# Kernel tuning notes

Measured on AMD Instinct MI355X. Metric: run time of the kernel, lower is better.

Reference implementation:

```python
import jax, jax.numpy as jnp
import numpy as np

N = 50000   # nodes
E = 800000  # edges
H = 3       # attention heads
IN_F = 128
HID = 128
NUM_CLASSES = 6
GAT_SLOPE = 0.2   # DGL GATConv internal leaky_relu slope
ACT_SLOPE = 0.01  # nn.LeakyReLU default


def setup_inputs() -> dict:
    key = jax.random.key(0)
    ks = jax.random.split(key, 24)
    s = 0.05
    inp = {
        "in_feat": jax.random.normal(ks[0], (N, IN_F), jnp.float32),
        "src": jax.random.randint(ks[1], (E,), 0, N, jnp.int32),
        "dst": jax.random.randint(ks[2], (E,), 0, N, jnp.int32),
        # GATConv 1: W (IN_F, H*HID), attn vectors (H, HID), bias (H*HID)
        "W1": jax.random.normal(ks[3], (IN_F, H * HID), jnp.float32) * s,
        "al1": jax.random.normal(ks[4], (H, HID), jnp.float32) * s,
        "ar1": jax.random.normal(ks[5], (H, HID), jnp.float32) * s,
        "b1": jnp.zeros((H * HID,), jnp.float32),
        # GATConv 2
        "W2": jax.random.normal(ks[6], (HID, H * HID), jnp.float32) * s,
        "al2": jax.random.normal(ks[7], (H, HID), jnp.float32) * s,
        "ar2": jax.random.normal(ks[8], (H, HID), jnp.float32) * s,
        "b2": jnp.zeros((H * HID,), jnp.float32),
    }
    # Dense MLP head lin1..lin4 (HID->HID) and lin5 (HID->NUM_CLASSES)
    for i in range(1, 5):
        inp[f"lw{i}"] = jax.random.normal(ks[8 + 2 * i], (HID, HID), jnp.float32) * s
        inp[f"lb{i}"] = jnp.zeros((HID,), jnp.float32)
    inp["lw5"] = jax.random.normal(ks[20], (HID, NUM_CLASSES), jnp.float32) * s
    inp["lb5"] = jnp.zeros((NUM_CLASSES,), jnp.float32)
    return inp


def gat_conv(x, src, dst, W, al, ar, b):
    # x: (N, F_in) -> out: (N, H, HID)
    h = (x @ W).reshape(N, H, HID)
    el = jnp.einsum('nhf,hf->nh', h, al)  # (N, H)
    er = jnp.einsum('nhf,hf->nh', h, ar)
    e = jax.nn.leaky_relu(el[src] + er[dst], GAT_SLOPE)  # (E, H)
    # edge softmax over incoming edges of each dst node
    m = jax.ops.segment_max(e, dst, num_segments=N)
    m = jnp.where(jnp.isfinite(m), m, 0.0)
    ex = jnp.exp(e - m[dst])
    denom = jax.ops.segment_sum(ex, dst, num_segments=N)
    alpha = ex / (denom[dst] + 1e-9)  # (E, H)
    out = jax.ops.segment_sum(alpha[:, :, None] * h[src], dst, num_segments=N)
    return out + b.reshape(1, H, HID)


def reference(in_feat, src, dst, W1, al1, ar1, b1, W2, al2, ar2, b2,
              lw1, lb1, lw2, lb2, lw3, lb3, lw4, lb4, lw5, lb5):
    act = lambda x: jax.nn.leaky_relu(x, ACT_SLOPE)
    h = act(gat_conv(in_feat, src, dst, W1, al1, ar1, b1)).mean(axis=1)
    h = act(gat_conv(h, src, dst, W2, al2, ar2, b2)).mean(axis=1)
    h = act(h @ lw1 + lb1)
    h = act(h @ lw2 + lb2)
    h = act(h @ lw3 + lb3)
    h = act(h @ lw4 + lb4)
    return h @ lw5 + lb5
```

## Files before the change

### kernel.cpp

```cpp
#include <hip/hip_runtime.h>
#include <hip/hip_bf16.h>


typedef __attribute__((ext_vector_type(8))) short short8;
typedef __attribute__((ext_vector_type(4))) float float4v;

__device__ inline short f2bf(float x) {
    union { float f; unsigned u; } v; v.f = x;
    unsigned r = v.u + 0x7FFFu + ((v.u >> 16) & 1u);
    return (short)(r >> 16);
}
__device__ inline float bf2f(short b) {
    union { float f; unsigned u; } v;
    v.u = ((unsigned)(unsigned short)b) << 16;
    return v.f;
}
__device__ inline short8 zero8() { short8 z = {0,0,0,0,0,0,0,0}; return z; }

#define BM 128
#define BN 128
#define BK 32
#define LSTR 40
#define MSTR 136
#define MROWS 64

__global__ void prep_kernel(
    const float* __restrict__ in_feat, short* __restrict__ P1h,
    short* __restrict__ P1l, int n4, int cb, int wb,
    const int* __restrict__ dst, int* __restrict__ cnt, int E,
    const float* __restrict__ w1, const float* __restrict__ w2,
    const float* __restrict__ m1, const float* __restrict__ m2,
    const float* __restrict__ m3, const float* __restrict__ m4,
    const float* __restrict__ w5,
    short* __restrict__ w1h, short* __restrict__ w1l,
    short* __restrict__ w2h, short* __restrict__ w2l,
    short* __restrict__ m1h, short* __restrict__ m1l,
    short* __restrict__ m2h, short* __restrict__ m2l,
    short* __restrict__ m3h, short* __restrict__ m3l,
    short* __restrict__ m4h, short* __restrict__ m4l,
    short* __restrict__ w5h, short* __restrict__ w5l)
{
    int blk = blockIdx.x;
    if (blk < cb) {
        int i = blk * 256 + threadIdx.x;
        if (i >= n4) return;
        float4 v = *(const float4*)(in_feat + (size_t)i * 4);
        float xs[4] = {v.x, v.y, v.z, v.w};
        short hs[4], ls[4];
        #pragma unroll
        for (int j = 0; j < 4; ++j) {
            hs[j] = f2bf(xs[j]);
            ls[j] = f2bf(xs[j] - bf2f(hs[j]));
        }
        *(uint2*)(P1h + (size_t)i * 4) = *(uint2*)hs;
        *(uint2*)(P1l + (size_t)i * 4) = *(uint2*)ls;
    } else if (blk < cb + wb) {
        int j = (blk - cb) * 256 + threadIdx.x;
        const float* src; short* th; short* tl; int Nc, base;
        if      (j < 49152)  { src = w1; th = w1h; tl = w1l; Nc = 384; base = 0; }
        else if (j < 98304)  { src = w2; th = w2h; tl = w2l; Nc = 384; base = 49152; }
        else if (j < 114688) { src = m1; th = m1h; tl = m1l; Nc = 128; base = 98304; }
        else if (j < 131072) { src = m2; th = m2h; tl = m2l; Nc = 128; base = 114688; }
        else if (j < 147456) { src = m3; th = m3h; tl = m3l; Nc = 128; base = 131072; }
        else if (j < 163840) { src = m4; th = m4h; tl = m4l; Nc = 128; base = 147456; }
        else if (j < 164608) { src = w5; th = w5h; tl = w5l; Nc = 6;   base = 163840; }
        else return;
        int i = j - base;
        int k = i / Nc, c = i - k * Nc;
        float v = src[i];
        short h = f2bf(v);
        th[(size_t)c * 128 + k] = h;
        tl[(size_t)c * 128 + k] = f2bf(v - bf2f(h));
    } else {
        int e = (blk - cb - wb) * 256 + threadIdx.x;
        if (e < E) atomicAdd(&cnt[dst[e]], 1);
    }
}

__global__ __launch_bounds__(256) void gemm_mfma(
    const short* __restrict__ Ahi, const short* __restrict__ Alo,
    const short* __restrict__ Bth, const short* __restrict__ Btl,
    const float* __restrict__ bias,
    float* __restrict__ Cf, short* __restrict__ Chi, short* __restrict__ Clo,
    float* __restrict__ el, float* __restrict__ er,
    const float* __restrict__ al, const float* __restrict__ ar,
    int M, int Nc, int flags)
{
    __shared__ short Ah[BM * LSTR], Al_[BM * LSTR];
    __shared__ short Bh[BN * LSTR], Bl_[BN * LSTR];

    int tid = threadIdx.x, lane = tid & 63, wave = tid >> 6;
    int l15 = lane & 15, q = lane >> 4;
    int rowBase = blockIdx.y * BM, colBase = blockIdx.x * BN;

    float4v acc[2][8];
    #pragma unroll
    for (int mt = 0; mt < 2; ++mt)
        #pragma unroll
        for (int nt = 0; nt < 8; ++nt)
            acc[mt][nt] = (float4v){0.f, 0.f, 0.f, 0.f};

    for (int k0 = 0; k0 < 128; k0 += BK) {
        #pragma unroll
        for (int s = 0; s < 2; ++s) {
            int c = tid + s * 256;
            int r = c >> 2, kq = (c & 3) * 8;
            int gr = rowBase + r;
            short8 vh = zero8(), vl = zero8();
            if (gr < M) {
                vh = *(const short8*)(Ahi + (size_t)gr * 128 + k0 + kq);
                vl = *(const short8*)(Alo + (size_t)gr * 128 + k0 + kq);
            }
            *(short8*)&Ah[r * LSTR + kq]  = vh;
            *(short8*)&Al_[r * LSTR + kq] = vl;
            int gc = colBase + r;
            short8 wh = zero8(), wl = zero8();
            if (gc < Nc) {
                wh = *(const short8*)(Bth + (size_t)gc * 128 + k0 + kq);
                wl = *(const short8*)(Btl + (size_t)gc * 128 + k0 + kq);
            }
            *(short8*)&Bh[r * LSTR + kq]  = wh;
            *(short8*)&Bl_[r * LSTR + kq] = wl;
        }
        __syncthreads();

        short8 aH[2], aL2[2];
        #pragma unroll
        for (int mt = 0; mt < 2; ++mt) {
            int off = (wave * 32 + mt * 16 + l15) * LSTR + q * 8;
            aH[mt]  = *(short8*)&Ah[off];
            aL2[mt] = *(short8*)&Al_[off];
        }
        #pragma unroll
        for (int nt = 0; nt < 8; ++nt) {
            int off = (nt * 16 + l15) * LSTR + q * 8;
            short8 bH = *(short8*)&Bh[off];
            short8 bL = *(short8*)&Bl_[off];
            #pragma unroll
            for (int mt = 0; mt < 2; ++mt) {
                acc[mt][nt] = __builtin_amdgcn_mfma_f32_16x16x32_bf16(aH[mt], bH, acc[mt][nt], 0, 0, 0);
                acc[mt][nt] = __builtin_amdgcn_mfma_f32_16x16x32_bf16(aH[mt], bL, acc[mt][nt], 0, 0, 0);
                acc[mt][nt] = __builtin_amdgcn_mfma_f32_16x16x32_bf16(aL2[mt], bH, acc[mt][nt], 0, 0, 0);
            }
        }
        __syncthreads();
    }

    if (flags & 4) {
        const float* alh = al + colBase;
        const float* arh = ar + colBase;
        float pel[2][4] = {}, per_[2][4] = {};
        #pragma unroll
        for (int nt = 0; nt < 8; ++nt) {
            float av = alh[nt * 16 + l15];
            float rv = arh[nt * 16 + l15];
            #pragma unroll
            for (int mt = 0; mt < 2; ++mt)
                #pragma unroll
                for (int i = 0; i < 4; ++i) {
                    pel[mt][i]  += acc[mt][nt][i] * av;
                    per_[mt][i] += acc[mt][nt][i] * rv;
                }
        }
        #pragma unroll
        for (int mask = 1; mask < 16; mask <<= 1)
            #pragma unroll
            for (int mt = 0; mt < 2; ++mt)
                #pragma unroll
                for (int i = 0; i < 4; ++i) {
                    pel[mt][i]  += __shfl_xor(pel[mt][i], mask);
                    per_[mt][i] += __shfl_xor(per_[mt][i], mask);
                }
        if (l15 == 0) {
            #pragma unroll
            for (int mt = 0; mt < 2; ++mt)
                #pragma unroll
                for (int i = 0; i < 4; ++i) {
                    int r = rowBase + wave * 32 + mt * 16 + q * 4 + i;
                    if (r < M) {
                        el[r * 3 + blockIdx.x] = pel[mt][i];
                        er[r * 3 + blockIdx.x] = per_[mt][i];
                    }
                }
        }
    }

    #pragma unroll
    for (int mt = 0; mt < 2; ++mt) {
        #pragma unroll
        for (int nt = 0; nt < 8; ++nt) {
            int c = colBase + nt * 16 + l15;
            if (c >= Nc) continue;
            float bv = (flags & 1) ? bias[c] : 0.f;
            #pragma unroll
            for (int i = 0; i < 4; ++i) {
                int r = rowBase + wave * 32 + mt * 16 + q * 4 + i;
                if (r >= M) continue;
                float v = acc[mt][nt][i] + bv;
                if (flags & 2) v = (v < 0.f) ? 0.01f * v : v;
                size_t idx = (size_t)r * Nc + c;
                if (flags & 8)  Cf[idx] = v;
                if (flags & 16) {
                    short hh = f2bf(v);
                    Chi[idx] = hh;
                    if (flags & 32) Clo[idx] = f2bf(v - bf2f(hh));
                }
            }
        }
    }
}

__global__ __launch_bounds__(256) void mlp_fused(
    const short* __restrict__ Ph, const short* __restrict__ Pl,
    const short* __restrict__ w1h, const short* __restrict__ w1l,
    const short* __restrict__ w2h, const short* __restrict__ w2l,
    const short* __restrict__ w3h, const short* __restrict__ w3l,
    const short* __restrict__ w4h, const short* __restrict__ w4l,
    const short* __restrict__ w5h, const short* __restrict__ w5l,
    const float* __restrict__ b1, const float* __restrict__ b2,
    const float* __restrict__ b3, const float* __restrict__ b4,
    const float* __restrict__ b5,
    float* __restrict__ out, int M)
{
    __shared__ short AH[MROWS * MSTR], AL[MROWS * MSTR];
    __shared__ short WH[128 * LSTR], WL[128 * LSTR];

    int tid = threadIdx.x, lane = tid & 63, wave = tid >> 6;
    int l15 = lane & 15, q = lane >> 4;
    int rowBase = blockIdx.x * MROWS;

    #pragma unroll
    for (int s = 0; s < 4; ++s) {
        int idx = tid + s * 256;
        int r = idx >> 4, kq = (idx & 15) * 8;
        int gr = rowBase + r;
        short8 vh = zero8(), vl = zero8();
        if (gr < M) {
            vh = *(const short8*)(Ph + (size_t)gr * 128 + kq);
            vl = *(const short8*)(Pl + (size_t)gr * 128 + kq);
        }
        *(short8*)&AH[r * MSTR + kq] = vh;
        *(short8*)&AL[r * MSTR + kq] = vl;
    }

    const short* Whs[4] = {w1h, w2h, w3h, w4h};
    const short* Wls[4] = {w1l, w2l, w3l, w4l};
    const float* Bss[4] = {b1, b2, b3, b4};

    #pragma unroll
    for (int L = 0; L < 4; ++L) {
        float4v acc[8];
        #pragma unroll
        for (int nt = 0; nt < 8; ++nt)
            acc[nt] = (float4v){0.f, 0.f, 0.f, 0.f};

        for (int k0 = 0; k0 < 128; k0 += BK) {
            #pragma unroll
            for (int s = 0; s < 4; ++s) {
                int idx = tid + s * 256;
                int plane = idx >> 9, rem = idx & 511;
                int c = rem >> 2, kq = (rem & 3) * 8;
                short8 v = *(const short8*)((plane ? Wls[L] : Whs[L]) +
                                            (size_t)c * 128 + k0 + kq);
                *(short8*)&((plane ? WL : WH)[c * LSTR + kq]) = v;
            }
            __syncthreads();
            int offa = (wave * 16 + l15) * MSTR + k0 + q * 8;
            short8 aH  = *(short8*)&AH[offa];
            short8 aL2 = *(short8*)&AL[offa];
            #pragma unroll
            for (int nt = 0; nt < 8; ++nt) {
                int off = (nt * 16 + l15) * LSTR + q * 8;
                short8 bH = *(short8*)&WH[off];
                short8 bL = *(short8*)&WL[off];
                acc[nt] = __builtin_amdgcn_mfma_f32_16x16x32_bf16(aH, bH, acc[nt], 0, 0, 0);
                acc[nt] = __builtin_amdgcn_mfma_f32_16x16x32_bf16(aH, bL, acc[nt], 0, 0, 0);
                acc[nt] = __builtin_amdgcn_mfma_f32_16x16x32_bf16(aL2, bH, acc[nt], 0, 0, 0);
            }
            __syncthreads();
        }
        #pragma unroll
        for (int nt = 0; nt < 8; ++nt) {
            int c = nt * 16 + l15;
            float bv = Bss[L][c];
            #pragma unroll
            for (int i = 0; i < 4; ++i) {
                int r = wave * 16 + q * 4 + i;
                float v = acc[nt][i] + bv;
                v = (v < 0.f) ? 0.01f * v : v;
                short hh = f2bf(v);
                AH[r * MSTR + c] = hh;
                AL[r * MSTR + c] = f2bf(v - bf2f(hh));
            }
        }
        __syncthreads();
    }

    float4v acc5 = (float4v){0.f, 0.f, 0.f, 0.f};
    for (int k0 = 0; k0 < 128; k0 += BK) {
        if (tid < 128) {
            int plane = tid >> 6, rem = tid & 63;
            int c = rem >> 2, kq = (rem & 3) * 8;
            short8 v = zero8();
            if (c < 6)
                v = *(const short8*)((plane ? w5l : w5h) + (size_t)c * 128 + k0 + kq);
            *(short8*)&((plane ? WL : WH)[c * LSTR + kq]) = v;
        }
        __syncthreads();
        int offa = (wave * 16 + l15) * MSTR + k0 + q * 8;
        short8 aH  = *(short8*)&AH[offa];
        short8 aL2 = *(short8*)&AL[offa];
        int offb = l15 * LSTR + q * 8;
        short8 bH = *(short8*)&WH[offb];
        short8 bL = *(short8*)&WL[offb];
        acc5 = __builtin_amdgcn_mfma_f32_16x16x32_bf16(aH, bH, acc5, 0, 0, 0);
        acc5 = __builtin_amdgcn_mfma_f32_16x16x32_bf16(aH, bL, acc5, 0, 0, 0);
        acc5 = __builtin_amdgcn_mfma_f32_16x16x32_bf16(aL2, bH, acc5, 0, 0, 0);
        __syncthreads();
    }
    if (l15 < 6) {
        float bv = b5[l15];
        #pragma unroll
        for (int i = 0; i < 4; ++i) {
            int r = rowBase + wave * 16 + q * 4 + i;
            if (r < M) out[(size_t)r * 6 + l15] = acc5[i] + bv;
        }
    }
}

__global__ __launch_bounds__(1024) void scan_block(const int* __restrict__ cnt,
                                                   int* __restrict__ off,
                                                   int* __restrict__ bsum, int n)
{
    __shared__ int tmp[1024];
    int tid = threadIdx.x;
    int i = blockIdx.x * 1024 + tid;
    int v = (i < n) ? cnt[i] : 0;
    tmp[tid] = v;
    __syncthreads();
    for (int s = 1; s < 1024; s <<= 1) {
        int t = (tid >= s) ? tmp[tid - s] : 0;
        __syncthreads();
        tmp[tid] += t;
        __syncthreads();
    }
    if (i < n) off[i] = tmp[tid] - v;
    if (tid == 1023) bsum[blockIdx.x] = tmp[1023];
}

__global__ void scan_add2(int* __restrict__ off, const int* __restrict__ bsum,
                          int n, int nb)
{
    __shared__ int pre[64];
    int tid = threadIdx.x;
    if (tid < 64) {
        int v = (tid < nb) ? bsum[tid] : 0;
        #pragma unroll
        for (int s = 1; s < 64; s <<= 1) {
            int t = __shfl_up(v, s);
            if (tid >= s) v += t;
        }
        pre[tid] = v;
    }
    __syncthreads();
    int i = blockIdx.x * blockDim.x + tid;
    if (i < n) {
        int chunk = i >> 10;
        off[i] += chunk ? pre[chunk - 1] : 0;
    }
    if (i == 0) off[n] = pre[nb - 1];
}

__global__ void scatter_kernel(const int* __restrict__ src, const int* __restrict__ dst,
                               const int* __restrict__ off, int* __restrict__ cnt,
                               int* __restrict__ csrc, int E)
{
    int e = blockIdx.x * blockDim.x + threadIdx.x;
    if (e < E) {
        int d = dst[e];
        int p = atomicSub(&cnt[d], 1) - 1;
        csrc[off[d] + p] = src[e];
    }
}

__global__ __launch_bounds__(192) void agg_kernel(
    const short* __restrict__ h, const float* __restrict__ el,
    const float* __restrict__ er, const int* __restrict__ off,
    const int* __restrict__ csrc, const float* __restrict__ bias,
    short* __restrict__ outH, short* __restrict__ outL, int N)
{
    int n = blockIdx.x;
    int tid = threadIdx.x;
    int head = tid >> 6;
    int l = tid & 63;
    int beg = off[n], end = off[n + 1];
    int deg = end - beg;

    __shared__ int   ssrc[64];
    __shared__ float sw[3][64];
    __shared__ float sm[384];

    int fbase = head * 128 + 2 * l;
    float erv = er[n * 3 + head];
    float ax = 0.f, ay = 0.f, den = 0.f, m_run = -1e30f;

    for (int base = 0; base < deg; base += 64) {
        int cnt = min(64, deg - base);
        if (tid < cnt) ssrc[tid] = csrc[beg + base + tid];
        __syncthreads();
        float e = -1e30f;
        if (l < cnt) {
            float t = el[ssrc[l] * 3 + head] + erv;
            e = (t < 0.f) ? 0.2f * t : t;
        }
        float mc = e;
        #pragma unroll
        for (int msk = 1; msk < 64; msk <<= 1) mc = fmaxf(mc, __shfl_xor(mc, msk));
        float m_new = fmaxf(m_run, mc);
        float scale = __expf(m_run - m_new);
        ax *= scale; ay *= scale; den *= scale;
        float w = (l < cnt) ? __expf(e - m_new) : 0.f;
        float wsum = w;
        #pragma unroll
        for (int msk = 1; msk < 64; msk <<= 1) wsum += __shfl_xor(wsum, msk);
        den += wsum;
        sw[head][l] = w;
        m_run = m_new;
        #pragma unroll 4
        for (int qq = 0; qq < cnt; ++qq) {
            int s = ssrc[qq];
            float w2 = sw[head][qq];
            unsigned v = *(const unsigned*)(h + (size_t)s * 384 + fbase);
            union { unsigned u; float f; } f0, f1;
            f0.u = v << 16; f1.u = v & 0xffff0000u;
            ax += w2 * f0.f;
            ay += w2 * f1.f;
        }
        __syncthreads();
    }
    float r = 1.f / (den + 1e-9f);
    if (deg == 0) r = 0.f;
    float2 bv = *(const float2*)(bias + fbase);
    float vx = ax * r + bv.x; vx = (vx < 0.f) ? 0.01f * vx : vx;
    float vy = ay * r + bv.y; vy = (vy < 0.f) ? 0.01f * vy : vy;
    sm[fbase]     = vx;
    sm[fbase + 1] = vy;
    __syncthreads();
    if (tid < 64) {
        int f0i = tid * 2, f1i = f0i + 1;
        float mx = (sm[f0i] + sm[128 + f0i] + sm[256 + f0i]) * (1.0f / 3.0f);
        float my = (sm[f1i] + sm[128 + f1i] + sm[256 + f1i]) * (1.0f / 3.0f);
        short hx = f2bf(mx), lx = f2bf(mx - bf2f(hx));
        short hy = f2bf(my), ly = f2bf(my - bf2f(hy));
        unsigned ph = (unsigned)(unsigned short)hx | ((unsigned)(unsigned short)hy << 16);
        unsigned pl = (unsigned)(unsigned short)lx | ((unsigned)(unsigned short)ly << 16);
        *(unsigned*)(outH + (size_t)n * 128 + f0i) = ph;
        *(unsigned*)(outL + (size_t)n * 128 + f0i) = pl;
    }
}

extern "C" void kernel_launch(void* const* d_in, const int* in_sizes, int n_in,
                              void* d_out, int out_size, void* d_ws, size_t ws_size,
                              hipStream_t stream)
{
    const float* in_feat = (const float*)d_in[0];
    const int*   src     = (const int*)d_in[1];
    const int*   dst     = (const int*)d_in[2];
    const float* W1  = (const float*)d_in[3];
    const float* al1 = (const float*)d_in[4];
    const float* ar1 = (const float*)d_in[5];
    const float* b1  = (const float*)d_in[6];
    const float* W2  = (const float*)d_in[7];
    const float* al2 = (const float*)d_in[8];
    const float* ar2 = (const float*)d_in[9];
    const float* b2  = (const float*)d_in[10];
    const float* lw1 = (const float*)d_in[11];
    const float* lb1 = (const float*)d_in[12];
    const float* lw2 = (const float*)d_in[13];
    const float* lb2 = (const float*)d_in[14];
    const float* lw3 = (const float*)d_in[15];
    const float* lb3 = (const float*)d_in[16];
    const float* lw4 = (const float*)d_in[17];
    const float* lb4 = (const float*)d_in[18];
    const float* lw5 = (const float*)d_in[19];
    const float* lb5 = (const float*)d_in[20];

    const int N = in_sizes[0] / 128;
    const int E = in_sizes[1];

    size_t o = 0;
    auto alloc = [&](size_t bytes) { size_t p = o; o = (o + bytes + 255) & ~(size_t)255; return p; };
    char* ws = (char*)d_ws;
    short* P1h = (short*)(ws + alloc((size_t)N * 128 * 2));
    short* P1l = (short*)(ws + alloc((size_t)N * 128 * 2));
    short* P2h = (short*)(ws + alloc((size_t)N * 128 * 2));
    short* P2l = (short*)(ws + alloc((size_t)N * 128 * 2));
    short* AbH = (short*)(ws + alloc((size_t)N * 384 * 2));
    float* el  = (float*)(ws + alloc((size_t)N * 3 * 4));
    float* er  = (float*)(ws + alloc((size_t)N * 3 * 4));
    int*   cnt  = (int*)(ws + alloc((size_t)N * 4));
    int*   off  = (int*)(ws + alloc((size_t)(N + 1) * 4));
    int*   bsum = (int*)(ws + alloc((size_t)4096));
    int*   csrc = (int*)(ws + alloc((size_t)E * 4));
    short* w1th = (short*)(ws + alloc((size_t)384 * 128 * 2));
    short* w1tl = (short*)(ws + alloc((size_t)384 * 128 * 2));
    short* w2th = (short*)(ws + alloc((size_t)384 * 128 * 2));
    short* w2tl = (short*)(ws + alloc((size_t)384 * 128 * 2));
    short* l1th = (short*)(ws + alloc((size_t)128 * 128 * 2));
    short* l1tl = (short*)(ws + alloc((size_t)128 * 128 * 2));
    short* l2th = (short*)(ws + alloc((size_t)128 * 128 * 2));
    short* l2tl = (short*)(ws + alloc((size_t)128 * 128 * 2));
    short* l3th = (short*)(ws + alloc((size_t)128 * 128 * 2));
    short* l3tl = (short*)(ws + alloc((size_t)128 * 128 * 2));
    short* l4th = (short*)(ws + alloc((size_t)128 * 128 * 2));
    short* l4tl = (short*)(ws + alloc((size_t)128 * 128 * 2));
    short* l5th = (short*)(ws + alloc((size_t)6 * 128 * 2));
    short* l5tl = (short*)(ws + alloc((size_t)6 * 128 * 2));
    (void)ws_size;

    float* out = (float*)d_out;

    hipMemsetAsync(cnt, 0, (size_t)N * 4, stream);
    int n4 = N * 128 / 4;
    int cb = (n4 + 255) / 256;
    int wb = (164608 + 255) / 256;
    int hb = (E + 255) / 256;
    prep_kernel<<<cb + wb + hb, 256, 0, stream>>>(
        in_feat, P1h, P1l, n4, cb, wb, dst, cnt, E,
        W1, W2, lw1, lw2, lw3, lw4, lw5,
        w1th, w1tl, w2th, w2tl, l1th, l1tl, l2th, l2tl,
        l3th, l3tl, l4th, l4tl, l5th, l5tl);

    int nb = (N + 1023) / 1024;
    scan_block<<<nb, 1024, 0, stream>>>(cnt, off, bsum, N);
    scan_add2<<<(N + 255) / 256, 256, 0, stream>>>(off, bsum, N, nb);
    scatter_kernel<<<(E + 255) / 256, 256, 0, stream>>>(src, dst, off, cnt, csrc, E);

    int RB = (N + BM - 1) / BM;
    auto gemm = [&](const short* ah, const short* alo, const short* bth, const short* btl,
                    const float* bias, float* cf, short* chi, short* clo,
                    float* elp, float* erp, const float* alp, const float* arp,
                    int Nc, int flags) {
        dim3 grid((Nc + BN - 1) / BN, RB);
        gemm_mfma<<<grid, 256, 0, stream>>>(ah, alo, bth, btl, bias, cf, chi, clo,
                                            elp, erp, alp, arp, N, Nc, flags);
    };

    gemm(P1h, P1l, w1th, w1tl, nullptr, nullptr, AbH, nullptr, el, er, al1, ar1, 384, 4 | 16);
    agg_kernel<<<N, 192, 0, stream>>>(AbH, el, er, off, csrc, b1, P2h, P2l, N);

    gemm(P2h, P2l, w2th, w2tl, nullptr, nullptr, AbH, nullptr, el, er, al2, ar2, 384, 4 | 16);
    agg_kernel<<<N, 192, 0, stream>>>(AbH, el, er, off, csrc, b2, P1h, P1l, N);

    int RBM = (N + MROWS - 1) / MROWS;
    mlp_fused<<<RBM, 256, 0, stream>>>(P1h, P1l,
                                       l1th, l1tl, l2th, l2tl, l3th, l3tl,
                                       l4th, l4tl, l5th, l5tl,
                                       lb1, lb2, lb3, lb4, lb5, out, N);
}
```

Measured before the change: 566.1 us.

## Interleave heads in GEMM output and aggregate one node per wavefront

A new GEMM output mode stores the projected features head-interleaved, as [node][feature][head], so each lane of the aggregation kernel reads all three heads for two features with a single 12-byte load. The aggregation kernel now gives each node one 64-lane wavefront and packs four nodes per 256-thread block. It keeps three online-softmax states per lane and computes the head mean in registers, which removes the block-wide __syncthreads and the shared-memory reduction. The cost is more registers per lane, a 12-byte load that is not 16-byte aligned, and tripled shuffle reductions per chunk.

```diff
diff --git a/kernel.cpp b/kernel.cpp
--- a/kernel.cpp
+++ b/kernel.cpp
@@ -14,6 +14,12 @@
     union { float f; unsigned u; } v;
     v.u = ((unsigned)(unsigned short)b) << 16;
     return v.f;
+}
+__device__ inline float bfhi(unsigned u) {
+    union { unsigned u; float f; } v; v.u = u & 0xffff0000u; return v.f;
+}
+__device__ inline float bflo(unsigned u) {
+    union { unsigned u; float f; } v; v.u = u << 16; return v.f;
 }
 __device__ inline short8 zero8() { short8 z = {0,0,0,0,0,0,0,0}; return z; }
 
@@ -198,9 +204,11 @@
                 if (r >= M) continue;
                 float v = acc[mt][nt][i] + bv;
                 if (flags & 2) v = (v < 0.f) ? 0.01f * v : v;
-                size_t idx = (size_t)r * Nc + c;
-                if (flags & 8)  Cf[idx] = v;
+                if (flags & 8)  Cf[(size_t)r * Nc + c] = v;
                 if (flags & 16) {
+                    size_t idx = (flags & 64)
+                        ? ((size_t)r * 128 + (size_t)(c - colBase)) * 3 + blockIdx.x
+                        : (size_t)r * Nc + c;
                     short hh = f2bf(v);
                     Chi[idx] = hh;
                     if (flags & 32) Clo[idx] = f2bf(v - bf2f(hh));
@@ -383,80 +391,93 @@
     }
 }
 
-__global__ __launch_bounds__(192) void agg_kernel(
+__global__ __launch_bounds__(256) void agg_kernel(
     const short* __restrict__ h, const float* __restrict__ el,
     const float* __restrict__ er, const int* __restrict__ off,
     const int* __restrict__ csrc, const float* __restrict__ bias,
     short* __restrict__ outH, short* __restrict__ outL, int N)
 {
-    int n = blockIdx.x;
-    int tid = threadIdx.x;
-    int head = tid >> 6;
-    int l = tid & 63;
+    int w = threadIdx.x >> 6;
+    int l = threadIdx.x & 63;
+    int n = blockIdx.x * 4 + w;
+    if (n >= N) return;
+
+    __shared__ int   ssrc[4][64];
+    __shared__ float sw3[4][64][3];
+
     int beg = off[n], end = off[n + 1];
     int deg = end - beg;
-
-    __shared__ int   ssrc[64];
-    __shared__ float sw[3][64];
-    __shared__ float sm[384];
-
-    int fbase = head * 128 + 2 * l;
-    float erv = er[n * 3 + head];
-    float ax = 0.f, ay = 0.f, den = 0.f, m_run = -1e30f;
+    float er0 = er[n * 3 + 0], er1 = er[n * 3 + 1], er2 = er[n * 3 + 2];
+
+    float a00 = 0.f, a01 = 0.f, a02 = 0.f;
+    float a10 = 0.f, a11 = 0.f, a12 = 0.f;
+    float den0 = 0.f, den1 = 0.f, den2 = 0.f;
+    float m0 = -1e30f, m1 = -1e30f, m2 = -1e30f;
 
     for (int base = 0; base < deg; base += 64) {
         int cnt = min(64, deg - base);
-        if (tid < cnt) ssrc[tid] = csrc[beg + base + tid];
-        __syncthreads();
-        float e = -1e30f;
+        if (l < cnt) ssrc[w][l] = csrc[beg + base + l];
+        float e0 = -1e30f, e1 = -1e30f, e2 = -1e30f;
         if (l < cnt) {
-            float t = el[ssrc[l] * 3 + head] + erv;
-            e = (t < 0.f) ? 0.2f * t : t;
-        }
-        float mc = e;
-        #pragma unroll
-        for (int msk = 1; msk < 64; msk <<= 1) mc = fmaxf(mc, __shfl_xor(mc, msk));
-        float m_new = fmaxf(m_run, mc);
-        float scale = __expf(m_run - m_new);
-        ax *= scale; ay *= scale; den *= scale;
-        float w = (l < cnt) ? __expf(e - m_new) : 0.f;
-        float wsum = w;
-        #pragma unroll
-        for (int msk = 1; msk < 64; msk <<= 1) wsum += __shfl_xor(wsum, msk);
-        den += wsum;
-        sw[head][l] = w;
-        m_run = m_new;
+            const float* ep = el + (size_t)ssrc[w][l] * 3;
+            float t0 = ep[0] + er0, t1 = ep[1] + er1, t2 = ep[2] + er2;
+            e0 = (t0 < 0.f) ? 0.2f * t0 : t0;
+            e1 = (t1 < 0.f) ? 0.2f * t1 : t1;
+            e2 = (t2 < 0.f) ? 0.2f * t2 : t2;
+        }
+        float c0 = e0, c1 = e1, c2 = e2;
+        #pragma unroll
+        for (int msk = 1; msk < 64; msk <<= 1) {
+            c0 = fmaxf(c0, __shfl_xor(c0, msk));
+            c1 = fmaxf(c1, __shfl_xor(c1, msk));
+            c2 = fmaxf(c2, __shfl_xor(c2, msk));
+        }
+        float n0 = fmaxf(m0, c0), n1 = fmaxf(m1, c1), n2 = fmaxf(m2, c2);
+        float s0 = __expf(m0 - n0), s1 = __expf(m1 - n1), s2 = __expf(m2 - n2);
+        a00 *= s0; a01 *= s1; a02 *= s2;
+        a10 *= s0; a11 *= s1; a12 *= s2;
+        den0 *= s0; den1 *= s1; den2 *= s2;
+        float w0 = (l < cnt) ? __expf(e0 - n0) : 0.f;
+        float w1 = (l < cnt) ? __expf(e1 - n1) : 0.f;
+        float w2 = (l < cnt) ? __expf(e2 - n2) : 0.f;
+        float ws0 = w0, ws1 = w1, ws2 = w2;
+        #pragma unroll
+        for (int msk = 1; msk < 64; msk <<= 1) {
+            ws0 += __shfl_xor(ws0, msk);
+            ws1 += __shfl_xor(ws1, msk);
+            ws2 += __shfl_xor(ws2, msk);
+        }
+        den0 += ws0; den1 += ws1; den2 += ws2;
+        sw3[w][l][0] = w0; sw3[w][l][1] = w1; sw3[w][l][2] = w2;
+        m0 = n0; m1 = n1; m2 = n2;
         #pragma unroll 4
         for (int qq = 0; qq < cnt; ++qq) {
-            int s = ssrc[qq];
-            float w2 = sw[head][qq];
-            unsigned v = *(const unsigned*)(h + (size_t)s * 384 + fbase);
-            union { unsigned u; float f; } f0, f1;
-            f0.u = v << 16; f1.u = v & 0xffff0000u;
-            ax += w2 * f0.f;
-            ay += w2 * f1.f;
-        }
-        __syncthreads();
-    }
-    float r = 1.f / (den + 1e-9f);
-    if (deg == 0) r = 0.f;
-    float2 bv = *(const float2*)(bias + fbase);
-    float vx = ax * r + bv.x; vx = (vx < 0.f) ? 0.01f * vx : vx;
-    float vy = ay * r + bv.y; vy = (vy < 0.f) ? 0.01f * vy : vy;
-    sm[fbase]     = vx;
-    sm[fbase + 1] = vy;
-    __syncthreads();
-    if (tid < 64) {
-        int f0i = tid * 2, f1i = f0i + 1;
-        float mx = (sm[f0i] + sm[128 + f0i] + sm[256 + f0i]) * (1.0f / 3.0f);
-        float my = (sm[f1i] + sm[128 + f1i] + sm[256 + f1i]) * (1.0f / 3.0f);
-        short hx = f2bf(mx), lx = f2bf(mx - bf2f(hx));
-        short hy = f2bf(my), ly = f2bf(my - bf2f(hy));
-        unsigned ph = (unsigned)(unsigned short)hx | ((unsigned)(unsigned short)hy << 16);
-        unsigned pl = (unsigned)(unsigned short)lx | ((unsigned)(unsigned short)ly << 16);
-        *(unsigned*)(outH + (size_t)n * 128 + f0i) = ph;
-        *(unsigned*)(outL + (size_t)n * 128 + f0i) = pl;
-    }
+            int s = ssrc[w][qq];
+            float q0 = sw3[w][qq][0], q1 = sw3[w][qq][1], q2 = sw3[w][qq][2];
+            uint3 v = *(const uint3*)(h + (size_t)s * 384 + l * 6);
+            a00 += q0 * bflo(v.x); a01 += q1 * bfhi(v.x); a02 += q2 * bflo(v.y);
+            a10 += q0 * bfhi(v.y); a11 += q1 * bflo(v.z); a12 += q2 * bfhi(v.z);
+        }
+    }
+    float r0 = 1.f / (den0 + 1e-9f), r1 = 1.f / (den1 + 1e-9f), r2 = 1.f / (den2 + 1e-9f);
+    if (deg == 0) { r0 = r1 = r2 = 0.f; }
+    int f0 = 2 * l, f1 = 2 * l + 1;
+    float b00 = bias[f0], b01 = bias[128 + f0], b02 = bias[256 + f0];
+    float b10 = bias[f1], b11 = bias[128 + f1], b12 = bias[256 + f1];
+    float v00 = a00 * r0 + b00; v00 = (v00 < 0.f) ? 0.01f * v00 : v00;
+    float v01 = a01 * r1 + b01; v01 = (v01 < 0.f) ? 0.01f * v01 : v01;
+    float v02 = a02 * r2 + b02; v02 = (v02 < 0.f) ? 0.01f * v02 : v02;
+    float v10 = a10 * r0 + b10; v10 = (v10 < 0.f) ? 0.01f * v10 : v10;
+    float v11 = a11 * r1 + b11; v11 = (v11 < 0.f) ? 0.01f * v11 : v11;
+    float v12 = a12 * r2 + b12; v12 = (v12 < 0.f) ? 0.01f * v12 : v12;
+    float mx = (v00 + v01 + v02) * (1.0f / 3.0f);
+    float my = (v10 + v11 + v12) * (1.0f / 3.0f);
+    short hx = f2bf(mx), lx = f2bf(mx - bf2f(hx));
+    short hy = f2bf(my), ly = f2bf(my - bf2f(hy));
+    unsigned ph = (unsigned)(unsigned short)hx | ((unsigned)(unsigned short)hy << 16);
+    unsigned pl = (unsigned)(unsigned short)lx | ((unsigned)(unsigned short)ly << 16);
+    *(unsigned*)(outH + (size_t)n * 128 + f0) = ph;
+    *(unsigned*)(outL + (size_t)n * 128 + f0) = pl;
 }
 
 extern "C" void kernel_launch(void* const* d_in, const int* in_sizes, int n_in,
@@ -545,12 +566,13 @@
         gemm_mfma<<<grid, 256, 0, stream>>>(ah, alo, bth, btl, bias, cf, chi, clo,
                                             elp, erp, alp, arp, N, Nc, flags);
     };
-
-    gemm(P1h, P1l, w1th, w1tl, nullptr, nullptr, AbH, nullptr, el, er, al1, ar1, 384, 4 | 16);
-    agg_kernel<<<N, 192, 0, stream>>>(AbH, el, er, off, csrc, b1, P2h, P2l, N);
-
-    gemm(P2h, P2l, w2th, w2tl, nullptr, nullptr, AbH, nullptr, el, er, al2, ar2, 384, 4 | 16);
-    agg_kernel<<<N, 192, 0, stream>>>(AbH, el, er, off, csrc, b2, P1h, P1l, N);
+    int aggGrid = (N + 3) / 4;
+
+    gemm(P1h, P1l, w1th, w1tl, nullptr, nullptr, AbH, nullptr, el, er, al1, ar1, 384, 4 | 16 | 64);
+    agg_kernel<<<aggGrid, 256, 0, stream>>>(AbH, el, er, off, csrc, b1, P2h, P2l, N);
+
+    gemm(P2h, P2l, w2th, w2tl, nullptr, nullptr, AbH, nullptr, el, er, al2, ar2, 384, 4 | 16 | 64);
+    agg_kernel<<<aggGrid, 256, 0, stream>>>(AbH, el, er, off, csrc, b2, P1h, P1l, N);
 
     int RBM = (N + MROWS - 1) / MROWS;
     mlp_fused<<<RBM, 256, 0, stream>>>(P1h, P1l,
```

Measured after the change: 567.8 us. Within noise of the previous version (+0.3%).
